# Kernel optimization log

Measured on AMD Instinct MI355X. Metric: run time of the kernel, lower is better.

## Reference

```python
import jax, jax.numpy as jnp
import numpy as np

BS, LX, LY, H, MD = 16, 1024, 1024, 512, 512


def setup_inputs() -> dict:
    key = jax.random.key(0)
    ks = jax.random.split(key, 8)
    x = jax.random.normal(ks[0], (BS, LX, H), dtype=jnp.float32)
    y = jax.random.normal(ks[1], (BS, LY, H), dtype=jnp.float32)
    y_mask = jax.random.bernoulli(ks[2], 0.2, (BS, LY))  # True = masked
    s1 = 1.0 / np.sqrt(H)
    W1 = jax.random.uniform(ks[3], (MD, H), jnp.float32, -s1, s1)
    b1 = jax.random.uniform(ks[4], (MD,), jnp.float32, -s1, s1)
    W2 = jax.random.uniform(ks[5], (MD, H), jnp.float32, -s1, s1)
    b2 = jax.random.uniform(ks[6], (MD,), jnp.float32, -s1, s1)
    s2 = 1.0 / np.sqrt(MD)
    k7, k8 = jax.random.split(ks[7])
    w_o = jax.random.uniform(k7, (MD,), jnp.float32, -s2, s2)
    b_o = jax.random.uniform(k8, (), jnp.float32, -s2, s2)
    return {"x": x, "y": y, "y_mask": y_mask, "W1": W1, "b1": b1,
            "W2": W2, "b2": b2, "w_o": w_o, "b_o": b_o}


def reference(x, y, y_mask, W1, b1, W2, b2, w_o, b_o):
    # Projections: [B,L,MD]
    x_proj = jax.nn.relu(jnp.einsum('blh,mh->blm', x, W1) + b1)
    y_proj = jax.nn.relu(jnp.einsum('blh,mh->blm', y, W2) + b2)
    # o_liner is linear, so o_liner(x_i + y_j) = w_o.x_i + w_o.y_j + b_o
    sx = x_proj @ w_o  # [B,Lx]
    sy = y_proj @ w_o  # [B,Ly]
    scores = sx[:, :, None] + sy[:, None, :] + b_o  # [B,Lx,Ly]
    scores = jnp.where(y_mask[:, None, :], jnp.float32(-1e7), scores)
    alpha = jax.nn.softmax(scores, axis=-1)  # softmax over len_y
    return alpha
```

## Files before the change

kernel.cpp:

```cpp
#include <hip/hip_runtime.h>
#include <hip/hip_bf16.h>

#define BS 16
#define LX 1024
#define LY 1024
#define H 512
#define MD 512
#define RY (BS * LY)

typedef __attribute__((ext_vector_type(8))) __bf16 bf16x8;
typedef __attribute__((ext_vector_type(4))) float floatx4;

__device__ __forceinline__ void load_lds16(const __bf16* g, __bf16* l) {
    __builtin_amdgcn_global_load_lds(
        (const __attribute__((address_space(1))) void*)g,
        (__attribute__((address_space(3))) void*)l,
        16, 0, 0);
}

__global__ __launch_bounds__(256) void prep_w2(const float* __restrict__ W2,
                                               __bf16* __restrict__ wb) {
    const int i = blockIdx.x * 256 + threadIdx.x;
    const float4 a = *(const float4*)(W2 + (size_t)i * 8);
    const float4 b = *(const float4*)(W2 + (size_t)i * 8 + 4);
    bf16x8 v = { (__bf16)a.x, (__bf16)a.y, (__bf16)a.z, (__bf16)a.w,
                 (__bf16)b.x, (__bf16)b.y, (__bf16)b.z, (__bf16)b.w };
    *(bf16x8*)(wb + (size_t)i * 8) = v;
}

#define BM 64
#define BN 128
#define BKT 64
#define ASTR 72
__global__ __launch_bounds__(256) void gemm_sy(const float* __restrict__ Y,
                                               const __bf16* __restrict__ wb,
                                               const float* __restrict__ b2,
                                               const float* __restrict__ wo,
                                               float* __restrict__ part) {
    __shared__ __align__(16) __bf16 As[BM * ASTR];
    __shared__ __align__(16) __bf16 Bs[BN * BKT];

    const int tid  = threadIdx.x;
    const int lane = tid & 63;
    const int wave = tid >> 6;
    const int wm = wave >> 1;
    const int wn = wave & 1;
    const int la = lane & 15;
    const int qa = lane >> 4;

    const int id = blockIdx.x;
    const int mt = ((id >> 5) << 3) | (id & 7);
    const int nt = (id >> 3) & 3;
    const int m0 = mt * BM, n0 = nt * BN;

    const int lrow = lane >> 3;
    const int lcol = ((lane & 7) ^ lrow) * 8;

    const int ar = tid >> 2;
    const int ac = (tid & 3) * 16;
    const float* ybase = Y + (size_t)(m0 + ar) * H + ac;

    floatx4 acc[2][4] = {};

    for (int k0 = 0; k0 < H; k0 += BKT) {
        __syncthreads();
        #pragma unroll
        for (int r = 0; r < 4; ++r) {
            const int rb = r * 32 + wave * 8;
            load_lds16(wb + (size_t)(n0 + rb + lrow) * H + k0 + lcol, &Bs[rb * BKT]);
        }
        const float4 a0 = *(const float4*)(ybase + k0);
        const float4 a1 = *(const float4*)(ybase + k0 + 4);
        const float4 a2 = *(const float4*)(ybase + k0 + 8);
        const float4 a3 = *(const float4*)(ybase + k0 + 12);
        bf16x8 p0 = { (__bf16)a0.x, (__bf16)a0.y, (__bf16)a0.z, (__bf16)a0.w,
                      (__bf16)a1.x, (__bf16)a1.y, (__bf16)a1.z, (__bf16)a1.w };
        bf16x8 p1 = { (__bf16)a2.x, (__bf16)a2.y, (__bf16)a2.z, (__bf16)a2.w,
                      (__bf16)a3.x, (__bf16)a3.y, (__bf16)a3.z, (__bf16)a3.w };
        *(bf16x8*)&As[ar * ASTR + ac]     = p0;
        *(bf16x8*)&As[ar * ASTR + ac + 8] = p1;
        __syncthreads();

        #pragma unroll
        for (int kh = 0; kh < 2; ++kh) {
            bf16x8 afr[2], bfr[4];
            #pragma unroll
            for (int mf = 0; mf < 2; ++mf)
                afr[mf] = *(const bf16x8*)&As[(wm * 32 + mf * 16 + la) * ASTR + kh * 32 + qa * 8];
            #pragma unroll
            for (int nf = 0; nf < 4; ++nf) {
                const int row  = wn * 64 + nf * 16 + la;
                const int slot = (kh * 4 + qa) ^ (la & 7);
                bfr[nf] = *(const bf16x8*)&Bs[row * BKT + slot * 8];
            }
            #pragma unroll
            for (int mf = 0; mf < 2; ++mf)
                #pragma unroll
                for (int nf = 0; nf < 4; ++nf)
                    acc[mf][nf] = __builtin_amdgcn_mfma_f32_16x16x32_bf16(afr[mf], bfr[nf], acc[mf][nf], 0, 0, 0);
        }
    }

    const int slice = nt * 2 + wn;
    #pragma unroll
    for (int mf = 0; mf < 2; ++mf) {
        #pragma unroll
        for (int reg = 0; reg < 4; ++reg) {
            float s = 0.f;
            #pragma unroll
            for (int nf = 0; nf < 4; ++nf) {
                const int n = n0 + wn * 64 + nf * 16 + la;
                float v = acc[mf][nf][reg] + b2[n];
                v = fmaxf(v, 0.f);
                s += v * wo[n];
            }
            s += __shfl_xor(s, 1);
            s += __shfl_xor(s, 2);
            s += __shfl_xor(s, 4);
            s += __shfl_xor(s, 8);
            if (la == 0) {
                const int m = m0 + wm * 32 + mf * 16 + qa * 4 + reg;
                part[(size_t)slice * RY + m] = s;
            }
        }
    }
}

__global__ __launch_bounds__(256) void softmax_bcast(const float* __restrict__ part,
                                                     const int* __restrict__ mask,
                                                     floatx4* __restrict__ out) {
    const int tid = threadIdx.x;
    const long base_row = (long)blockIdx.x * 16;
    const int b = (int)(base_row >> 10);
    __shared__ float red[8];

    float vx = 0.f, vy = 0.f, vz = 0.f, vw = 0.f;
    #pragma unroll
    for (int t = 0; t < 8; ++t) {
        const float4 q = *(const float4*)(part + (size_t)t * RY + b * LY + tid * 4);
        vx += q.x; vy += q.y; vz += q.z; vw += q.w;
    }
    const int4 m4 = *(const int4*)(mask + b * LY + tid * 4);

    float mx = -INFINITY;
    if (!m4.x) mx = vx;
    if (!m4.y) mx = fmaxf(mx, vy);
    if (!m4.z) mx = fmaxf(mx, vz);
    if (!m4.w) mx = fmaxf(mx, vw);
    #pragma unroll
    for (int off = 1; off < 64; off <<= 1) mx = fmaxf(mx, __shfl_xor(mx, off));
    if ((tid & 63) == 0) red[tid >> 6] = mx;
    __syncthreads();
    mx = fmaxf(fmaxf(red[0], red[1]), fmaxf(red[2], red[3]));

    floatx4 e;
    e.x = m4.x ? 0.f : __expf(vx - mx);
    e.y = m4.y ? 0.f : __expf(vy - mx);
    e.z = m4.z ? 0.f : __expf(vz - mx);
    e.w = m4.w ? 0.f : __expf(vw - mx);
    float sum = e.x + e.y + e.z + e.w;
    #pragma unroll
    for (int off = 1; off < 64; off <<= 1) sum += __shfl_xor(sum, off);
    if ((tid & 63) == 0) red[4 + (tid >> 6)] = sum;
    __syncthreads();
    sum = red[4] + red[5] + red[6] + red[7];
    const float inv = 1.0f / sum;
    e.x *= inv; e.y *= inv; e.z *= inv; e.w *= inv;

    floatx4* o = out + base_row * (LY / 4) + tid;
    #pragma unroll
    for (int r = 0; r < 16; ++r)
        __builtin_nontemporal_store(e, o + r * (LY / 4));
}

extern "C" void kernel_launch(void* const* d_in, const int* in_sizes, int n_in,
                              void* d_out, int out_size, void* d_ws, size_t ws_size,
                              hipStream_t stream) {
    const float* y  = (const float*)d_in[1];
    const int*   ym = (const int*)  d_in[2];
    const float* W2 = (const float*)d_in[5];
    const float* b2 = (const float*)d_in[6];
    const float* wo = (const float*)d_in[7];

    char* ws = (char*)d_ws;
    __bf16* wb   = (__bf16*)ws;
    float*  part = (float*)(ws + (size_t)MD * H * 2);

    prep_w2<<<(MD * H) / (256 * 8), 256, 0, stream>>>(W2, wb);
    gemm_sy<<<(MD / BN) * (RY / BM), 256, 0, stream>>>(y, wb, b2, wo, part);
    softmax_bcast<<<(BS * LX) / 16, 256, 0, stream>>>(part, ym, (floatx4*)d_out);
}
```

Before: 142.4 us.

## Fuse softmax broadcast into GEMM via per-batch atomic counter barrier

Merges the separate softmax/broadcast kernel into the GEMM kernel. Each block, after writing its partial sy scores, increments a per-batch counter and spins until all 64 blocks of that batch have finished, then computes the masked softmax and writes 16 output rows. This removes one kernel launch and lets output stores from finished batches overlap GEMM work on other batches. In exchange it relies on all blocks of a batch being co-resident to avoid deadlock, and it adds spin-wait and an occupancy hint via launch bounds.

```diff
diff --git a/kernel.cpp b/kernel.cpp
--- a/kernel.cpp
+++ b/kernel.cpp
@@ -19,8 +19,10 @@
 }
 
 __global__ __launch_bounds__(256) void prep_w2(const float* __restrict__ W2,
-                                               __bf16* __restrict__ wb) {
+                                               __bf16* __restrict__ wb,
+                                               int* __restrict__ cnt) {
     const int i = blockIdx.x * 256 + threadIdx.x;
+    if (blockIdx.x == 0 && threadIdx.x < BS) cnt[threadIdx.x] = 0;
     const float4 a = *(const float4*)(W2 + (size_t)i * 8);
     const float4 b = *(const float4*)(W2 + (size_t)i * 8 + 4);
     bf16x8 v = { (__bf16)a.x, (__bf16)a.y, (__bf16)a.z, (__bf16)a.w,
@@ -32,11 +34,14 @@
 #define BN 128
 #define BKT 64
 #define ASTR 72
-__global__ __launch_bounds__(256) void gemm_sy(const float* __restrict__ Y,
-                                               const __bf16* __restrict__ wb,
-                                               const float* __restrict__ b2,
-                                               const float* __restrict__ wo,
-                                               float* __restrict__ part) {
+__global__ __launch_bounds__(256, 4) void gemm_smax(const float* __restrict__ Y,
+                                                    const __bf16* __restrict__ wb,
+                                                    const float* __restrict__ b2,
+                                                    const float* __restrict__ wo,
+                                                    float* __restrict__ part,
+                                                    const int* __restrict__ mask,
+                                                    floatx4* __restrict__ out,
+                                                    int* __restrict__ cnt) {
     __shared__ __align__(16) __bf16 As[BM * ASTR];
     __shared__ __align__(16) __bf16 Bs[BN * BKT];
 
@@ -124,15 +129,25 @@
             }
         }
     }
-}
-
-__global__ __launch_bounds__(256) void softmax_bcast(const float* __restrict__ part,
-                                                     const int* __restrict__ mask,
-                                                     floatx4* __restrict__ out) {
-    const int tid = threadIdx.x;
-    const long base_row = (long)blockIdx.x * 16;
-    const int b = (int)(base_row >> 10);
-    __shared__ float red[8];
+
+    const int b = mt >> 4;
+    const int rk = ((mt & 15) << 2) | nt;
+    __syncthreads();
+    if (tid == 0) {
+        __threadfence();
+        atomicAdd(&cnt[b], 1);
+    }
+    if (tid == 0) {
+        int tries = 0;
+        while (__hip_atomic_load(&cnt[b], __ATOMIC_ACQUIRE, __HIP_MEMORY_SCOPE_AGENT) < 64) {
+            __builtin_amdgcn_s_sleep(8);
+            if (++tries > (1 << 26)) break;
+        }
+    }
+    __syncthreads();
+
+    float* red = (float*)As;
+    const long base_row = (long)b * LX + (long)rk * 16;
 
     float vx = 0.f, vy = 0.f, vz = 0.f, vw = 0.f;
     #pragma unroll
@@ -185,8 +200,9 @@
     char* ws = (char*)d_ws;
     __bf16* wb   = (__bf16*)ws;
     float*  part = (float*)(ws + (size_t)MD * H * 2);
-
-    prep_w2<<<(MD * H) / (256 * 8), 256, 0, stream>>>(W2, wb);
-    gemm_sy<<<(MD / BN) * (RY / BM), 256, 0, stream>>>(y, wb, b2, wo, part);
-    softmax_bcast<<<(BS * LX) / 16, 256, 0, stream>>>(part, ym, (floatx4*)d_out);
-}
+    int*    cnt  = (int*)(part + 8 * RY);
+
+    prep_w2<<<(MD * H) / (256 * 8), 256, 0, stream>>>(W2, wb, cnt);
+    gemm_smax<<<(MD / BN) * (RY / BM), 256, 0, stream>>>(y, wb, b2, wo, part, ym,
+                                                         (floatx4*)d_out, cnt);
+}
```

Result: slower. 240.4 us (+68.8%).
